# Kernel optimization log

Measured on AMD Instinct MI355X. Metric: run time of the kernel, lower is better.

Reference implementation:

```python
import jax, jax.numpy as jnp
import numpy as np

N, C, H = 384, 128, 4

def setup_inputs() -> dict:
    key = jax.random.key(0)
    ks = jax.random.split(key, 8)
    s = 1.0 / np.sqrt(C).astype(np.float32)
    pair = jax.random.normal(ks[0], (N, N, C), jnp.float32)
    mask = (jax.random.uniform(ks[1], (N, N)) > 0.5).astype(jnp.float32)
    return {
        'pair': pair,
        'mask': mask,
        'ln_w': jnp.ones((C,), jnp.float32),
        'ln_b': jnp.zeros((C,), jnp.float32),
        'bias_w': jax.random.normal(ks[2], (H, C), jnp.float32) * s,
        'q_w': jax.random.normal(ks[3], (C, C), jnp.float32) * s,
        'k_w': jax.random.normal(ks[4], (C, C), jnp.float32) * s,
        'v_w': jax.random.normal(ks[5], (C, C), jnp.float32) * s,
        'g_w': jax.random.normal(ks[6], (C, C), jnp.float32) * s,
        'o_w': jax.random.normal(ks[7], (C, C), jnp.float32) * s,
    }

def reference(pair, mask, ln_w, ln_b, bias_w, q_w, k_w, v_w, g_w, o_w):
    n, _, c = pair.shape
    h = bias_w.shape[0]
    d = c // h  # qkv_dim = c_pair // num_head
    # LayerNorm over channel dim (eps=1e-5, torch default)
    mu = jnp.mean(pair, axis=-1, keepdims=True)
    var = jnp.var(pair, axis=-1, keepdims=True)
    x = (pair - mu) * jax.lax.rsqrt(var + 1e-5) * ln_w + ln_b  # [N,N,C]
    # nonbatched pair bias: Linear(C->H), then permute(2,0,1) -> [H,N,N]
    bias = jnp.einsum('ijc,hc->hij', x, bias_w)
    # per-row (b) attention over keys j; Linear weight W: y = x @ W.T
    q = (x @ q_w.T).reshape(n, n, h, d)
    k = (x @ k_w.T).reshape(n, n, h, d)
    v = (x @ v_w.T).reshape(n, n, h, d)
    mask_bias = 1e9 * (mask - 1.0)  # [N,N]: -inf-like where masked per row b, key j
    logits = jnp.einsum('bihd,bjhd->bhij', q, k) * (1.0 / np.sqrt(d).astype(np.float32))
    logits = logits + bias[None, :, :, :] + mask_bias[:, None, None, :]
    w = jax.nn.softmax(logits, axis=-1)  # [N,H,N,N]
    o = jnp.einsum('bhij,bjhd->bihd', w, v).reshape(n, n, c)
    gate = jax.nn.sigmoid(x @ g_w.T)
    return (gate * o) @ o_w.T  # [N,N,C]
```

## Files before the change

### kernel.cpp

```cpp
#include <hip/hip_runtime.h>
#include <hip/hip_bf16.h>

#define NN 384
#define CC 128
#define HH 4
#define QK_SCALE 0.17677669529663687f

typedef float f32x4 __attribute__((ext_vector_type(4)));
typedef short s16x8 __attribute__((ext_vector_type(8)));
typedef short s16x4 __attribute__((ext_vector_type(4)));
typedef unsigned short u16;
typedef unsigned int u32;

__device__ __forceinline__ u16 f2b(float f) {
  union { float f; u32 u; } c; c.f = f;
  u32 u = c.u + 0x7FFFu + ((c.u >> 16) & 1u);
  return (u16)(u >> 16);
}
__device__ __forceinline__ u32 pack2(float a, float b) {
  return (u32)f2b(a) | ((u32)f2b(b) << 16);
}
__device__ __forceinline__ u32 pack2t(float a, float b) {
  union { float f; u32 u; } x, y; x.f = a; y.f = b;
  return (x.u >> 16) | (y.u & 0xFFFF0000u);
}
__device__ __forceinline__ float b2f_lo(u32 u) {
  union { u32 u; float f; } c; c.u = u << 16; return c.f;
}
__device__ __forceinline__ float b2f_hi(u32 u) {
  union { u32 u; float f; } c; c.u = u & 0xFFFF0000u; return c.f;
}
__device__ __forceinline__ s16x4 mk4(u32 a, u32 b) {
  union { u32 u[2]; s16x4 v; } c; c.u[0] = a; c.u[1] = b; return c.v;
}

#define MFMA32(a, b, c) __builtin_amdgcn_mfma_f32_16x16x32_bf16((a), (b), (c), 0, 0, 0)
#define MFMA16(a, b, c) __builtin_amdgcn_mfma_f32_16x16x16bf16_1k((a), (b), (c), 0, 0, 0)

__global__ __launch_bounds__(256) void k_ln_bias(
    const float* __restrict__ pair, const float* __restrict__ ln_w,
    const float* __restrict__ ln_b, const float* __restrict__ bias_w,
    const float* __restrict__ q_w, const float* __restrict__ k_w,
    const float* __restrict__ v_w, const float* __restrict__ g_w,
    const float* __restrict__ o_w, u16* __restrict__ xb,
    u16* __restrict__ biasf, u16* __restrict__ wqk, u16* __restrict__ wv,
    u16* __restrict__ wg, u16* __restrict__ wo) {
  if (blockIdx.x == 36864) {
    const int t = threadIdx.x;
    const float2* q2 = (const float2*)q_w;
    const float2* k2 = (const float2*)k_w;
    const float2* v2 = (const float2*)v_w;
    const float2* g2 = (const float2*)g_w;
    const float2* o2 = (const float2*)o_w;
    u32* dq = (u32*)wqk;
    u32* dk = (u32*)wqk + 8192;
    u32* dv = (u32*)wv;
    u32* dg = (u32*)wg;
    u32* dw = (u32*)wo;
    for (int i = t; i < 8192; i += 256) {
      float2 a = q2[i];
      dq[i] = pack2(a.x * QK_SCALE, a.y * QK_SCALE);
      a = k2[i]; dk[i] = pack2(a.x, a.y);
      a = v2[i]; dv[i] = pack2(a.x, a.y);
      a = g2[i]; dg[i] = pack2(a.x, a.y);
      a = o2[i]; dw[i] = pack2(a.x, a.y);
    }
    return;
  }
  const int wave = threadIdx.x >> 6;
  const int l = threadIdx.x & 63;
  const int p = blockIdx.x * 4 + wave;

  const float2 v = ((const float2*)pair)[(size_t)p * 64 + l];
  float s = v.x + v.y, sq = v.x * v.x + v.y * v.y;
#pragma unroll
  for (int off = 32; off >= 1; off >>= 1) {
    s += __shfl_xor(s, off);
    sq += __shfl_xor(sq, off);
  }
  const float mean = s * (1.0f / 128.0f);
  const float rstd = rsqrtf(sq * (1.0f / 128.0f) - mean * mean + 1e-5f);
  const float2 lw = ((const float2*)ln_w)[l];
  const float2 lb2 = ((const float2*)ln_b)[l];
  const float x0 = (v.x - mean) * rstd * lw.x + lb2.x;
  const float x1 = (v.y - mean) * rstd * lw.y + lb2.y;
  ((u32*)xb)[(size_t)p * 64 + l] = pack2(x0, x1);

  const int i = p / NN;
  const int j = p - i * NN;
  const int slot = ((j & 12) << 4) + ((i & 15) << 2) + (j & 3);
#pragma unroll
  for (int h = 0; h < HH; ++h) {
    const float2 bw = ((const float2*)bias_w)[h * 64 + l];
    float bp = x0 * bw.x + x1 * bw.y;
#pragma unroll
    for (int off = 32; off >= 1; off >>= 1) bp += __shfl_xor(bp, off);
    if (l == 0)
      biasf[(((h * 24 + (j >> 4)) * 24 + (i >> 4)) << 8) + slot] = f2b(bp);
  }
}

__global__ __launch_bounds__(256) void k_qkv(
    const u16* __restrict__ xb, const u16* __restrict__ wqk,
    const u16* __restrict__ wv, u16* __restrict__ qg, u16* __restrict__ kg,
    u16* __restrict__ vtf) {
  const int bid = blockIdx.x;
  const int b = bid / 6, jt6 = bid % 6;
  const int jrow0 = b * NN + jt6 * 64, jloc0 = jt6 * 64;
  const int t = threadIdx.x, w = t >> 6, l = t & 63;
  const int lr = l & 15, lg = l >> 4;
  const int n0 = w * 64;
  const int m0v = (w & 1) * 2;
  const int n0v = (w >> 1) * 64;

  f32x4 acc[4][4];
  f32x4 accv[2][4];
#pragma unroll
  for (int a = 0; a < 4; ++a)
#pragma unroll
    for (int c = 0; c < 4; ++c) acc[a][c] = (f32x4){0.f, 0.f, 0.f, 0.f};
#pragma unroll
  for (int a = 0; a < 2; ++a)
#pragma unroll
    for (int c = 0; c < 4; ++c) accv[a][c] = (f32x4){0.f, 0.f, 0.f, 0.f};

#pragma unroll
  for (int cs = 0; cs < 4; ++cs) {
    s16x8 bx[4];
#pragma unroll
    for (int ms = 0; ms < 4; ++ms)
      bx[ms] = *(const s16x8*)&xb[(size_t)(jrow0 + ms * 16 + lr) * CC +
                                  cs * 32 + lg * 8];
#pragma unroll
    for (int ns = 0; ns < 4; ++ns) {
      const s16x8 aW =
          *(const s16x8*)&wqk[(n0 + ns * 16 + lr) * CC + cs * 32 + lg * 8];
#pragma unroll
      for (int ms = 0; ms < 4; ++ms)
        acc[ns][ms] = MFMA32(aW, bx[ms], acc[ns][ms]);
      const s16x8 bV =
          *(const s16x8*)&wv[(n0v + ns * 16 + lr) * CC + cs * 32 + lg * 8];
#pragma unroll
      for (int mv = 0; mv < 2; ++mv)
        accv[mv][ns] = MFMA32(bx[m0v + mv], bV, accv[mv][ns]);
    }
  }

  {
    u16* base = (n0 >= 128) ? kg : qg;
    const int nb = n0 & 64;
#pragma unroll
    for (int ns = 0; ns < 4; ++ns) {
      const int nl = nb + ns * 16 + lg * 4;
      const int h = nl >> 5, d0 = nl & 31;
#pragma unroll
      for (int ms = 0; ms < 4; ++ms) {
        u32* dst = (u32*)(base + (size_t)(b * 4 + h) * 12288 +
                          (jloc0 + ms * 16 + lr) * 32 + d0);
        dst[0] = pack2(acc[ns][ms][0], acc[ns][ms][1]);
        dst[1] = pack2(acc[ns][ms][2], acc[ns][ms][3]);
      }
    }
  }

#pragma unroll
  for (int mv = 0; mv < 2; ++mv) {
#pragma unroll
    for (int ns = 0; ns < 4; ++ns) {
      const int n = n0v + ns * 16 + lr;
      const int h = n >> 5;
      const int dt = (n >> 4) & 1;
      const int j0 = jloc0 + (m0v + mv) * 16;
      u32* dst = (u32*)vtf +
                 ((((size_t)(b * 4 + h)) * 24 + (j0 >> 4)) * 2 + dt) * 128 +
                 l * 2;
      dst[0] = pack2(accv[mv][ns][0], accv[mv][ns][1]);
      dst[1] = pack2(accv[mv][ns][2], accv[mv][ns][3]);
    }
  }
}

__global__ __launch_bounds__(256) void k_attn(
    const u16* __restrict__ qg, const u16* __restrict__ kg,
    const u16* __restrict__ vtf, const u16* __restrict__ biasf,
    const float* __restrict__ mask, float* __restrict__ io) {
  __shared__ float mb[NN];
  const int bid = blockIdx.x;
  const int bh = bid >> 1, half = bid & 1;
  const int b = bh >> 2, h = bh & 3;
  const int t = threadIdx.x, w = t >> 6, l = t & 63;
  const int lr = l & 15, lg = l >> 4;

  for (int i = t; i < NN; i += 256) mb[i] = 1e9f * (mask[b * NN + i] - 1.0f);
  __syncthreads();

  const int q0 = half * 192 + w * 48, it0 = q0 >> 4;
  const u16* qb = qg + (size_t)bh * 12288;
  const u16* kb = kg + (size_t)bh * 12288;
  const u32* vt = (const u32*)vtf + (size_t)bh * 6144;
  const u32* bbf = (const u32*)biasf + (size_t)h * 73728;

  s16x8 bQ[3];
#pragma unroll
  for (int ms = 0; ms < 3; ++ms)
    bQ[ms] = *(const s16x8*)&qb[(q0 + ms * 16 + lr) * 32 + lg * 8];

  float mr[3], ls[3];
  f32x4 oa[3][2];
#pragma unroll
  for (int ms = 0; ms < 3; ++ms) {
    mr[ms] = -3.0e38f;
    ls[ms] = 0.f;
    oa[ms][0] = (f32x4){0.f, 0.f, 0.f, 0.f};
    oa[ms][1] = (f32x4){0.f, 0.f, 0.f, 0.f};
  }
  const f32x4 z4 = {0.f, 0.f, 0.f, 0.f};

#pragma unroll
  for (int kt = 0; kt < 6; ++kt) {
    s16x8 aK[4];
#pragma unroll
    for (int js = 0; js < 4; ++js)
      aK[js] = *(const s16x8*)&kb[(kt * 64 + js * 16 + lr) * 32 + lg * 8];
    u32 bw[3][4][2];
#pragma unroll
    for (int ms = 0; ms < 3; ++ms)
#pragma unroll
      for (int js = 0; js < 4; ++js) {
        const u32* p = bbf + ((kt * 4 + js) * 24 + it0 + ms) * 128 + l * 2;
        bw[ms][js][0] = p[0];
        bw[ms][js][1] = p[1];
      }
    s16x4 aV[4][2];
#pragma unroll
    for (int st = 0; st < 4; ++st)
#pragma unroll
      for (int ns = 0; ns < 2; ++ns)
        aV[st][ns] =
            *(const s16x4*)(vt + ((kt * 4 + st) * 2 + ns) * 128 + l * 2);

    f32x4 sT[3][4];
#pragma unroll
    for (int ms = 0; ms < 3; ++ms)
#pragma unroll
      for (int js = 0; js < 4; ++js) sT[ms][js] = MFMA32(aK[js], bQ[ms], z4);

#pragma unroll
    for (int js = 0; js < 4; ++js) {
      const int jb = kt * 64 + js * 16 + lg * 4;
      const f32x4 m4 = *(const f32x4*)&mb[jb];
#pragma unroll
      for (int ms = 0; ms < 3; ++ms) {
        const u32 b0 = bw[ms][js][0], b1 = bw[ms][js][1];
        sT[ms][js][0] += b2f_lo(b0) + m4[0];
        sT[ms][js][1] += b2f_hi(b0) + m4[1];
        sT[ms][js][2] += b2f_lo(b1) + m4[2];
        sT[ms][js][3] += b2f_hi(b1) + m4[3];
      }
    }

    u32 pk[3][4][2];
#pragma unroll
    for (int ms = 0; ms < 3; ++ms) {
      float tm = -3.0e38f;
#pragma unroll
      for (int js = 0; js < 4; ++js)
#pragma unroll
        for (int r = 0; r < 4; ++r) tm = fmaxf(tm, sT[ms][js][r]);
      tm = fmaxf(tm, __shfl_xor(tm, 16));
      tm = fmaxf(tm, __shfl_xor(tm, 32));
      const float nm = fmaxf(mr[ms], tm);
      const float sc = __expf(mr[ms] - nm);
      mr[ms] = nm;
      float ts = 0.f;
#pragma unroll
      for (int js = 0; js < 4; ++js)
#pragma unroll
        for (int r = 0; r < 4; ++r) {
          const float p = __expf(sT[ms][js][r] - nm);
          sT[ms][js][r] = p;
          ts += p;
        }
      ts += __shfl_xor(ts, 16);
      ts += __shfl_xor(ts, 32);
      ls[ms] = ls[ms] * sc + ts;
      oa[ms][0] *= sc;
      oa[ms][1] *= sc;
#pragma unroll
      for (int js = 0; js < 4; ++js) {
        pk[ms][js][0] = pack2t(sT[ms][js][0], sT[ms][js][1]);
        pk[ms][js][1] = pack2t(sT[ms][js][2], sT[ms][js][3]);
      }
    }

#pragma unroll
    for (int st = 0; st < 4; ++st) {
#pragma unroll
      for (int ms = 0; ms < 3; ++ms) {
        const s16x4 pb = mk4(pk[ms][st][0], pk[ms][st][1]);
#pragma unroll
        for (int ns = 0; ns < 2; ++ns)
          oa[ms][ns] = MFMA16(aV[st][ns], pb, oa[ms][ns]);
      }
    }
  }

#pragma unroll
  for (int ms = 0; ms < 3; ++ms) {
    const float inv = 1.0f / ls[ms];
    float* orow = io + ((size_t)b * NN + q0 + ms * 16 + lr) * CC + h * 32;
#pragma unroll
    for (int ns = 0; ns < 2; ++ns) {
      f32x4 vo = oa[ms][ns];
      vo *= inv;
      *(f32x4*)&orow[ns * 16 + lg * 4] = vo;
    }
  }
}

__global__ __launch_bounds__(256) void k_gate_out(
    const u16* __restrict__ xb, const u16* __restrict__ wg,
    const u16* __restrict__ wo, float* __restrict__ io) {
  const int bid = blockIdx.x;
  const int t = threadIdx.x, w = t >> 6, l = t & 63;
  const int lr = l & 15, lg = l >> 4;
  const int m0g = bid * 64 + w * 16;

  f32x4 a1[8];
#pragma unroll
  for (int ns = 0; ns < 8; ++ns) a1[ns] = (f32x4){0.f, 0.f, 0.f, 0.f};
#pragma unroll
  for (int cs = 0; cs < 4; ++cs) {
    const s16x8 bx =
        *(const s16x8*)&xb[(size_t)(m0g + lr) * CC + cs * 32 + lg * 8];
#pragma unroll
    for (int ns = 0; ns < 8; ++ns) {
      const s16x8 aW =
          *(const s16x8*)&wg[(ns * 16 + lr) * CC + cs * 32 + lg * 8];
      a1[ns] = MFMA32(aW, bx, a1[ns]);
    }
  }

  s16x4 pk2[8];
#pragma unroll
  for (int ns = 0; ns < 8; ++ns) {
    const f32x4 ov =
        *(const f32x4*)&io[(size_t)(m0g + lr) * CC + ns * 16 + lg * 4];
    float av[4];
#pragma unroll
    for (int r = 0; r < 4; ++r)
      av[r] = ov[r] / (1.0f + __expf(-a1[ns][r]));
    pk2[ns] = mk4(pack2(av[0], av[1]), pack2(av[2], av[3]));
  }

  f32x4 a2[8];
#pragma unroll
  for (int ns = 0; ns < 8; ++ns) a2[ns] = (f32x4){0.f, 0.f, 0.f, 0.f};
#pragma unroll
  for (int cs = 0; cs < 8; ++cs) {
#pragma unroll
    for (int ns = 0; ns < 8; ++ns) {
      const s16x4 aW2 =
          *(const s16x4*)&wo[(ns * 16 + lr) * CC + cs * 16 + lg * 4];
      a2[ns] = MFMA16(aW2, pk2[cs], a2[ns]);
    }
  }
#pragma unroll
  for (int ns = 0; ns < 8; ++ns)
    *(f32x4*)&io[(size_t)(m0g + lr) * CC + ns * 16 + lg * 4] = a2[ns];
}

extern "C" void kernel_launch(void* const* d_in, const int* in_sizes, int n_in,
                              void* d_out, int out_size, void* d_ws,
                              size_t ws_size, hipStream_t stream) {
  const float* pair = (const float*)d_in[0];
  const float* mask = (const float*)d_in[1];
  const float* ln_w = (const float*)d_in[2];
  const float* ln_b = (const float*)d_in[3];
  const float* bias_w = (const float*)d_in[4];
  const float* q_w = (const float*)d_in[5];
  const float* k_w = (const float*)d_in[6];
  const float* v_w = (const float*)d_in[7];
  const float* g_w = (const float*)d_in[8];
  const float* o_w = (const float*)d_in[9];

  char* wsb = (char*)d_ws;
  u16* xb = (u16*)wsb;
  u16* biasf = (u16*)(wsb + 37748736);
  u16* wqk = (u16*)(wsb + 38928384);
  u16* wv = (u16*)(wsb + 38993920);
  u16* wg = (u16*)(wsb + 39026688);
  u16* wo = (u16*)(wsb + 39059456);
  u16* qg = (u16*)(wsb + 39092224);
  u16* kg = (u16*)(wsb + 76840960);
  u16* vtf = (u16*)(wsb + 114589696);
  float* io = (float*)d_out;

  hipLaunchKernelGGL(k_ln_bias, dim3(NN * NN / 4 + 1), dim3(256), 0, stream,
                     pair, ln_w, ln_b, bias_w, q_w, k_w, v_w, g_w, o_w, xb,
                     biasf, wqk, wv, wg, wo);
  hipLaunchKernelGGL(k_qkv, dim3(NN * 6), dim3(256), 0, stream, xb, wqk, wv,
                     qg, kg, vtf);
  hipLaunchKernelGGL(k_attn, dim3(NN * HH * 2), dim3(256), 0, stream, qg, kg,
                     vtf, biasf, mask, io);
  hipLaunchKernelGGL(k_gate_out, dim3(NN * NN / 64), dim3(256), 0, stream, xb,
                     wg, wo, io);
}
```

Before: 620.5 us.

## Fuse QKV projection, attention, gating and output projection into one kernel

New measurement: 570.9 us. 1.09x faster.

```diff
diff --git a/kernel.cpp b/kernel.cpp
--- a/kernel.cpp
+++ b/kernel.cpp
@@ -5,6 +5,8 @@
 #define CC 128
 #define HH 4
 #define QK_SCALE 0.17677669529663687f
+#define LOG2E 1.4426950408889634f
+#define SMAX 20.0f
 
 typedef float f32x4 __attribute__((ext_vector_type(4)));
 typedef short s16x8 __attribute__((ext_vector_type(8)));
@@ -57,9 +59,10 @@
     u32* dv = (u32*)wv;
     u32* dg = (u32*)wg;
     u32* dw = (u32*)wo;
+    const float qs = QK_SCALE * LOG2E;
     for (int i = t; i < 8192; i += 256) {
       float2 a = q2[i];
-      dq[i] = pack2(a.x * QK_SCALE, a.y * QK_SCALE);
+      dq[i] = pack2(a.x * qs, a.y * qs);
       a = k2[i]; dk[i] = pack2(a.x, a.y);
       a = v2[i]; dv[i] = pack2(a.x, a.y);
       a = g2[i]; dg[i] = pack2(a.x, a.y);
@@ -96,278 +99,274 @@
 #pragma unroll
     for (int off = 32; off >= 1; off >>= 1) bp += __shfl_xor(bp, off);
     if (l == 0)
-      biasf[(((h * 24 + (j >> 4)) * 24 + (i >> 4)) << 8) + slot] = f2b(bp);
+      biasf[(((h * 24 + (j >> 4)) * 24 + (i >> 4)) << 8) + slot] =
+          f2b(bp * LOG2E);
   }
 }
 
-__global__ __launch_bounds__(256) void k_qkv(
+__global__ __launch_bounds__(256, 2) void k_mega(
     const u16* __restrict__ xb, const u16* __restrict__ wqk,
-    const u16* __restrict__ wv, u16* __restrict__ qg, u16* __restrict__ kg,
-    u16* __restrict__ vtf) {
+    const u16* __restrict__ wv, const u16* __restrict__ wg,
+    const u16* __restrict__ wo, const u16* __restrict__ biasf,
+    const float* __restrict__ mask, float* __restrict__ io) {
+  __shared__ u16 q_lds[192 * 40];
+  __shared__ u16 k_lds[192 * 40];
+  __shared__ u16 vt_lds[24 * 320];
+  __shared__ float mb[NN];
+
   const int bid = blockIdx.x;
-  const int b = bid / 6, jt6 = bid % 6;
-  const int jrow0 = b * NN + jt6 * 64, jloc0 = jt6 * 64;
+  const int b = bid >> 1, half = bid & 1;
   const int t = threadIdx.x, w = t >> 6, l = t & 63;
   const int lr = l & 15, lg = l >> 4;
-  const int n0 = w * 64;
-  const int m0v = (w & 1) * 2;
-  const int n0v = (w >> 1) * 64;
-
-  f32x4 acc[4][4];
-  f32x4 accv[2][4];
-#pragma unroll
-  for (int a = 0; a < 4; ++a)
-#pragma unroll
-    for (int c = 0; c < 4; ++c) acc[a][c] = (f32x4){0.f, 0.f, 0.f, 0.f};
-#pragma unroll
-  for (int a = 0; a < 2; ++a)
-#pragma unroll
-    for (int c = 0; c < 4; ++c) accv[a][c] = (f32x4){0.f, 0.f, 0.f, 0.f};
-
-#pragma unroll
-  for (int cs = 0; cs < 4; ++cs) {
-    s16x8 bx[4];
-#pragma unroll
-    for (int ms = 0; ms < 4; ++ms)
-      bx[ms] = *(const s16x8*)&xb[(size_t)(jrow0 + ms * 16 + lr) * CC +
-                                  cs * 32 + lg * 8];
-#pragma unroll
-    for (int ns = 0; ns < 4; ++ns) {
-      const s16x8 aW =
-          *(const s16x8*)&wqk[(n0 + ns * 16 + lr) * CC + cs * 32 + lg * 8];
-#pragma unroll
-      for (int ms = 0; ms < 4; ++ms)
-        acc[ns][ms] = MFMA32(aW, bx[ms], acc[ns][ms]);
-      const s16x8 bV =
-          *(const s16x8*)&wv[(n0v + ns * 16 + lr) * CC + cs * 32 + lg * 8];
-#pragma unroll
-      for (int mv = 0; mv < 2; ++mv)
-        accv[mv][ns] = MFMA32(bx[m0v + mv], bV, accv[mv][ns]);
+
+  for (int i = t; i < NN; i += 256)
+    mb[i] = LOG2E * 1e9f * (mask[b * NN + i] - 1.0f) - SMAX;
+
+  const int xrow_b = b * NN;
+  const int qrow_loc = half * 192 + w * 48;
+  const int itg0 = qrow_loc >> 4;
+  const f32x4 z4 = {0.f, 0.f, 0.f, 0.f};
+
+  u32 gos[3][HH][2][2];
+  s16x8 bQ[3];
+  float ls[3];
+  f32x4 oa[3][2];
+  u32 gatepk[3][2][2];
+
+#pragma unroll
+  for (int h = 0; h < HH; ++h) {
+    __syncthreads();
+
+    {
+      s16x8 bx[3][4];
+#pragma unroll
+      for (int ms = 0; ms < 3; ++ms)
+#pragma unroll
+        for (int cs = 0; cs < 4; ++cs)
+          bx[ms][cs] = *(const s16x8*)&xb[(size_t)(xrow_b + qrow_loc + ms * 16 +
+                                                   lr) * CC + cs * 32 + lg * 8];
+      f32x4 aq[2][3], ag[2][3];
+#pragma unroll
+      for (int ns = 0; ns < 2; ++ns)
+#pragma unroll
+        for (int ms = 0; ms < 3; ++ms) { aq[ns][ms] = z4; ag[ns][ms] = z4; }
+#pragma unroll
+      for (int cs = 0; cs < 4; ++cs) {
+#pragma unroll
+        for (int ns = 0; ns < 2; ++ns) {
+          const s16x8 aqw = *(const s16x8*)&wqk[(h * 32 + ns * 16 + lr) * CC +
+                                                cs * 32 + lg * 8];
+          const s16x8 agw = *(const s16x8*)&wg[(h * 32 + ns * 16 + lr) * CC +
+                                               cs * 32 + lg * 8];
+#pragma unroll
+          for (int ms = 0; ms < 3; ++ms) {
+            aq[ns][ms] = MFMA32(aqw, bx[ms][cs], aq[ns][ms]);
+            ag[ns][ms] = MFMA32(agw, bx[ms][cs], ag[ns][ms]);
+          }
+        }
+      }
+#pragma unroll
+      for (int ns = 0; ns < 2; ++ns)
+#pragma unroll
+        for (int ms = 0; ms < 3; ++ms) {
+          u32* dq = (u32*)q_lds + (w * 48 + ms * 16 + lr) * 20 + ns * 8 + lg * 2;
+          dq[0] = pack2(aq[ns][ms][0], aq[ns][ms][1]);
+          dq[1] = pack2(aq[ns][ms][2], aq[ns][ms][3]);
+          float sg[4];
+#pragma unroll
+          for (int r = 0; r < 4; ++r)
+            sg[r] = __builtin_amdgcn_rcpf(1.0f + __expf(-ag[ns][ms][r]));
+          gatepk[ms][ns][0] = pack2(sg[0], sg[1]);
+          gatepk[ms][ns][1] = pack2(sg[2], sg[3]);
+        }
+    }
+
+#pragma unroll
+    for (int ms = 0; ms < 3; ++ms) {
+      ls[ms] = 0.f;
+      oa[ms][0] = z4;
+      oa[ms][1] = z4;
+    }
+    const u32* bbf = (const u32*)biasf + (size_t)h * 73728;
+
+#pragma unroll
+    for (int c = 0; c < 2; ++c) {
+      if (c == 1) __syncthreads();
+      {
+        s16x8 bx2[3][4];
+#pragma unroll
+        for (int ms = 0; ms < 3; ++ms)
+#pragma unroll
+          for (int cs = 0; cs < 4; ++cs)
+            bx2[ms][cs] =
+                *(const s16x8*)&xb[(size_t)(xrow_b + c * 192 + w * 48 +
+                                            ms * 16 + lr) * CC + cs * 32 + lg * 8];
+        f32x4 ak2[2][3], av2[2][3];
+#pragma unroll
+        for (int ns = 0; ns < 2; ++ns)
+#pragma unroll
+          for (int ms = 0; ms < 3; ++ms) { ak2[ns][ms] = z4; av2[ns][ms] = z4; }
+#pragma unroll
+        for (int cs = 0; cs < 4; ++cs) {
+#pragma unroll
+          for (int ns = 0; ns < 2; ++ns) {
+            const s16x8 akw =
+                *(const s16x8*)&wqk[(128 + h * 32 + ns * 16 + lr) * CC +
+                                    cs * 32 + lg * 8];
+            const s16x8 avw = *(const s16x8*)&wv[(h * 32 + ns * 16 + lr) * CC +
+                                                 cs * 32 + lg * 8];
+#pragma unroll
+            for (int ms = 0; ms < 3; ++ms) {
+              ak2[ns][ms] = MFMA32(akw, bx2[ms][cs], ak2[ns][ms]);
+              av2[ns][ms] = MFMA32(avw, bx2[ms][cs], av2[ns][ms]);
+            }
+          }
+        }
+#pragma unroll
+        for (int ns = 0; ns < 2; ++ns)
+#pragma unroll
+          for (int ms = 0; ms < 3; ++ms) {
+            u32* dk = (u32*)k_lds + (w * 48 + ms * 16 + lr) * 20 + ns * 8 + lg * 2;
+            dk[0] = pack2(ak2[ns][ms][0], ak2[ns][ms][1]);
+            dk[1] = pack2(ak2[ns][ms][2], ak2[ns][ms][3]);
+            const int tt = (w * 3 + ms) * 2 + ns;
+#pragma unroll
+            for (int r = 0; r < 4; ++r)
+              vt_lds[tt * 320 + (lg * 4 + r) * 20 + lr] = f2b(av2[ns][ms][r]);
+          }
+      }
+      __syncthreads();
+
+      if (c == 0) {
+#pragma unroll
+        for (int ms = 0; ms < 3; ++ms)
+          bQ[ms] = *(const s16x8*)&q_lds[(w * 48 + ms * 16 + lr) * 40 + lg * 8];
+      }
+
+#pragma unroll
+      for (int ktl = 0; ktl < 3; ++ktl) {
+        const int ktg = c * 3 + ktl;
+        s16x8 aK[4];
+#pragma unroll
+        for (int js = 0; js < 4; ++js)
+          aK[js] =
+              *(const s16x8*)&k_lds[(ktl * 64 + js * 16 + lr) * 40 + lg * 8];
+        u32 bw[3][4][2];
+#pragma unroll
+        for (int ms = 0; ms < 3; ++ms)
+#pragma unroll
+          for (int js = 0; js < 4; ++js) {
+            const u32* p = bbf + ((ktg * 4 + js) * 24 + itg0 + ms) * 128 + l * 2;
+            bw[ms][js][0] = p[0];
+            bw[ms][js][1] = p[1];
+          }
+        s16x4 aV[4][2];
+#pragma unroll
+        for (int st = 0; st < 4; ++st)
+#pragma unroll
+          for (int ns = 0; ns < 2; ++ns)
+            aV[st][ns] = *(const s16x4*)&vt_lds[((ktl * 4 + st) * 2 + ns) * 320 +
+                                                lr * 20 + lg * 4];
+
+        f32x4 sT[3][4];
+#pragma unroll
+        for (int ms = 0; ms < 3; ++ms)
+#pragma unroll
+          for (int js = 0; js < 4; ++js) sT[ms][js] = MFMA32(aK[js], bQ[ms], z4);
+
+#pragma unroll
+        for (int js = 0; js < 4; ++js) {
+          const int jb = c * 192 + ktl * 64 + js * 16 + lg * 4;
+          const f32x4 m4 = *(const f32x4*)&mb[jb];
+#pragma unroll
+          for (int ms = 0; ms < 3; ++ms) {
+            const u32 b0 = bw[ms][js][0], b1 = bw[ms][js][1];
+            sT[ms][js][0] += b2f_lo(b0) + m4[0];
+            sT[ms][js][1] += b2f_hi(b0) + m4[1];
+            sT[ms][js][2] += b2f_lo(b1) + m4[2];
+            sT[ms][js][3] += b2f_hi(b1) + m4[3];
+          }
+        }
+
+        u32 pk[3][4][2];
+#pragma unroll
+        for (int ms = 0; ms < 3; ++ms) {
+          float ts = 0.f;
+#pragma unroll
+          for (int js = 0; js < 4; ++js)
+#pragma unroll
+            for (int r = 0; r < 4; ++r) {
+              const float p = exp2f(sT[ms][js][r]);
+              sT[ms][js][r] = p;
+              ts += p;
+            }
+          ts += __shfl_xor(ts, 16);
+          ts += __shfl_xor(ts, 32);
+          ls[ms] += ts;
+#pragma unroll
+          for (int js = 0; js < 4; ++js) {
+            pk[ms][js][0] = pack2t(sT[ms][js][0], sT[ms][js][1]);
+            pk[ms][js][1] = pack2t(sT[ms][js][2], sT[ms][js][3]);
+          }
+        }
+
+#pragma unroll
+        for (int st = 0; st < 4; ++st)
+#pragma unroll
+          for (int ms = 0; ms < 3; ++ms) {
+            const s16x4 pb = mk4(pk[ms][st][0], pk[ms][st][1]);
+#pragma unroll
+            for (int ns = 0; ns < 2; ++ns)
+              oa[ms][ns] = MFMA16(aV[st][ns], pb, oa[ms][ns]);
+          }
+      }
+    }
+
+#pragma unroll
+    for (int ms = 0; ms < 3; ++ms) {
+      const float inv = __builtin_amdgcn_rcpf(ls[ms]);
+#pragma unroll
+      for (int ns = 0; ns < 2; ++ns) {
+        const float g0 = b2f_lo(gatepk[ms][ns][0]);
+        const float g1 = b2f_hi(gatepk[ms][ns][0]);
+        const float g2 = b2f_lo(gatepk[ms][ns][1]);
+        const float g3 = b2f_hi(gatepk[ms][ns][1]);
+        const float v0 = oa[ms][ns][0] * inv * g0;
+        const float v1 = oa[ms][ns][1] * inv * g1;
+        const float v2 = oa[ms][ns][2] * inv * g2;
+        const float v3 = oa[ms][ns][3] * inv * g3;
+        gos[ms][h][ns][0] = pack2(v0, v1);
+        gos[ms][h][ns][1] = pack2(v2, v3);
+      }
     }
   }
 
-  {
-    u16* base = (n0 >= 128) ? kg : qg;
-    const int nb = n0 & 64;
-#pragma unroll
-    for (int ns = 0; ns < 4; ++ns) {
-      const int nl = nb + ns * 16 + lg * 4;
-      const int h = nl >> 5, d0 = nl & 31;
-#pragma unroll
-      for (int ms = 0; ms < 4; ++ms) {
-        u32* dst = (u32*)(base + (size_t)(b * 4 + h) * 12288 +
-                          (jloc0 + ms * 16 + lr) * 32 + d0);
-        dst[0] = pack2(acc[ns][ms][0], acc[ns][ms][1]);
-        dst[1] = pack2(acc[ns][ms][2], acc[ns][ms][3]);
-      }
-    }
+  f32x4 acc2[8][3];
+#pragma unroll
+  for (int ns2 = 0; ns2 < 8; ++ns2)
+#pragma unroll
+    for (int ms = 0; ms < 3; ++ms) acc2[ns2][ms] = z4;
+#pragma unroll
+  for (int h2 = 0; h2 < HH; ++h2)
+#pragma unroll
+    for (int ns = 0; ns < 2; ++ns)
+#pragma unroll
+      for (int ns2 = 0; ns2 < 8; ++ns2) {
+        const s16x4 aW = *(const s16x4*)&wo[(ns2 * 16 + lr) * CC + h2 * 32 +
+                                            ns * 16 + lg * 4];
+#pragma unroll
+        for (int ms = 0; ms < 3; ++ms)
+          acc2[ns2][ms] =
+              MFMA16(aW, mk4(gos[ms][h2][ns][0], gos[ms][h2][ns][1]),
+                     acc2[ns2][ms]);
+      }
+#pragma unroll
+  for (int ms = 0; ms < 3; ++ms) {
+    float* orow = io + (size_t)(xrow_b + qrow_loc + ms * 16 + lr) * CC;
+#pragma unroll
+    for (int ns2 = 0; ns2 < 8; ++ns2)
+      *(f32x4*)&orow[ns2 * 16 + lg * 4] = acc2[ns2][ms];
   }
-
-#pragma unroll
-  for (int mv = 0; mv < 2; ++mv) {
-#pragma unroll
-    for (int ns = 0; ns < 4; ++ns) {
-      const int n = n0v + ns * 16 + lr;
-      const int h = n >> 5;
-      const int dt = (n >> 4) & 1;
-      const int j0 = jloc0 + (m0v + mv) * 16;
-      u32* dst = (u32*)vtf +
-                 ((((size_t)(b * 4 + h)) * 24 + (j0 >> 4)) * 2 + dt) * 128 +
-                 l * 2;
-      dst[0] = pack2(accv[mv][ns][0], accv[mv][ns][1]);
-      dst[1] = pack2(accv[mv][ns][2], accv[mv][ns][3]);
-    }
-  }
-}
-
-__global__ __launch_bounds__(256) void k_attn(
-    const u16* __restrict__ qg, const u16* __restrict__ kg,
-    const u16* __restrict__ vtf, const u16* __restrict__ biasf,
-    const float* __restrict__ mask, float* __restrict__ io) {
-  __shared__ float mb[NN];
-  const int bid = blockIdx.x;
-  const int bh = bid >> 1, half = bid & 1;
-  const int b = bh >> 2, h = bh & 3;
-  const int t = threadIdx.x, w = t >> 6, l = t & 63;
-  const int lr = l & 15, lg = l >> 4;
-
-  for (int i = t; i < NN; i += 256) mb[i] = 1e9f * (mask[b * NN + i] - 1.0f);
-  __syncthreads();
-
-  const int q0 = half * 192 + w * 48, it0 = q0 >> 4;
-  const u16* qb = qg + (size_t)bh * 12288;
-  const u16* kb = kg + (size_t)bh * 12288;
-  const u32* vt = (const u32*)vtf + (size_t)bh * 6144;
-  const u32* bbf = (const u32*)biasf + (size_t)h * 73728;
-
-  s16x8 bQ[3];
-#pragma unroll
-  for (int ms = 0; ms < 3; ++ms)
-    bQ[ms] = *(const s16x8*)&qb[(q0 + ms * 16 + lr) * 32 + lg * 8];
-
-  float mr[3], ls[3];
-  f32x4 oa[3][2];
-#pragma unroll
-  for (int ms = 0; ms < 3; ++ms) {
-    mr[ms] = -3.0e38f;
-    ls[ms] = 0.f;
-    oa[ms][0] = (f32x4){0.f, 0.f, 0.f, 0.f};
-    oa[ms][1] = (f32x4){0.f, 0.f, 0.f, 0.f};
-  }
-  const f32x4 z4 = {0.f, 0.f, 0.f, 0.f};
-
-#pragma unroll
-  for (int kt = 0; kt < 6; ++kt) {
-    s16x8 aK[4];
-#pragma unroll
-    for (int js = 0; js < 4; ++js)
-      aK[js] = *(const s16x8*)&kb[(kt * 64 + js * 16 + lr) * 32 + lg * 8];
-    u32 bw[3][4][2];
-#pragma unroll
-    for (int ms = 0; ms < 3; ++ms)
-#pragma unroll
-      for (int js = 0; js < 4; ++js) {
-        const u32* p = bbf + ((kt * 4 + js) * 24 + it0 + ms) * 128 + l * 2;
-        bw[ms][js][0] = p[0];
-        bw[ms][js][1] = p[1];
-      }
-    s16x4 aV[4][2];
-#pragma unroll
-    for (int st = 0; st < 4; ++st)
-#pragma unroll
-      for (int ns = 0; ns < 2; ++ns)
-        aV[st][ns] =
-            *(const s16x4*)(vt + ((kt * 4 + st) * 2 + ns) * 128 + l * 2);
-
-    f32x4 sT[3][4];
-#pragma unroll
-    for (int ms = 0; ms < 3; ++ms)
-#pragma unroll
-      for (int js = 0; js < 4; ++js) sT[ms][js] = MFMA32(aK[js], bQ[ms], z4);
-
-#pragma unroll
-    for (int js = 0; js < 4; ++js) {
-      const int jb = kt * 64 + js * 16 + lg * 4;
-      const f32x4 m4 = *(const f32x4*)&mb[jb];
-#pragma unroll
-      for (int ms = 0; ms < 3; ++ms) {
-        const u32 b0 = bw[ms][js][0], b1 = bw[ms][js][1];
-        sT[ms][js][0] += b2f_lo(b0) + m4[0];
-        sT[ms][js][1] += b2f_hi(b0) + m4[1];
-        sT[ms][js][2] += b2f_lo(b1) + m4[2];
-        sT[ms][js][3] += b2f_hi(b1) + m4[3];
-      }
-    }
-
-    u32 pk[3][4][2];
-#pragma unroll
-    for (int ms = 0; ms < 3; ++ms) {
-      float tm = -3.0e38f;
-#pragma unroll
-      for (int js = 0; js < 4; ++js)
-#pragma unroll
-        for (int r = 0; r < 4; ++r) tm = fmaxf(tm, sT[ms][js][r]);
-      tm = fmaxf(tm, __shfl_xor(tm, 16));
-      tm = fmaxf(tm, __shfl_xor(tm, 32));
-      const float nm = fmaxf(mr[ms], tm);
-      const float sc = __expf(mr[ms] - nm);
-      mr[ms] = nm;
-      float ts = 0.f;
-#pragma unroll
-      for (int js = 0; js < 4; ++js)
-#pragma unroll
-        for (int r = 0; r < 4; ++r) {
-          const float p = __expf(sT[ms][js][r] - nm);
-          sT[ms][js][r] = p;
-          ts += p;
-        }
-      ts += __shfl_xor(ts, 16);
-      ts += __shfl_xor(ts, 32);
-      ls[ms] = ls[ms] * sc + ts;
-      oa[ms][0] *= sc;
-      oa[ms][1] *= sc;
-#pragma unroll
-      for (int js = 0; js < 4; ++js) {
-        pk[ms][js][0] = pack2t(sT[ms][js][0], sT[ms][js][1]);
-        pk[ms][js][1] = pack2t(sT[ms][js][2], sT[ms][js][3]);
-      }
-    }
-
-#pragma unroll
-    for (int st = 0; st < 4; ++st) {
-#pragma unroll
-      for (int ms = 0; ms < 3; ++ms) {
-        const s16x4 pb = mk4(pk[ms][st][0], pk[ms][st][1]);
-#pragma unroll
-        for (int ns = 0; ns < 2; ++ns)
-          oa[ms][ns] = MFMA16(aV[st][ns], pb, oa[ms][ns]);
-      }
-    }
-  }
-
-#pragma unroll
-  for (int ms = 0; ms < 3; ++ms) {
-    const float inv = 1.0f / ls[ms];
-    float* orow = io + ((size_t)b * NN + q0 + ms * 16 + lr) * CC + h * 32;
-#pragma unroll
-    for (int ns = 0; ns < 2; ++ns) {
-      f32x4 vo = oa[ms][ns];
-      vo *= inv;
-      *(f32x4*)&orow[ns * 16 + lg * 4] = vo;
-    }
-  }
-}
-
-__global__ __launch_bounds__(256) void k_gate_out(
-    const u16* __restrict__ xb, const u16* __restrict__ wg,
-    const u16* __restrict__ wo, float* __restrict__ io) {
-  const int bid = blockIdx.x;
-  const int t = threadIdx.x, w = t >> 6, l = t & 63;
-  const int lr = l & 15, lg = l >> 4;
-  const int m0g = bid * 64 + w * 16;
-
-  f32x4 a1[8];
-#pragma unroll
-  for (int ns = 0; ns < 8; ++ns) a1[ns] = (f32x4){0.f, 0.f, 0.f, 0.f};
-#pragma unroll
-  for (int cs = 0; cs < 4; ++cs) {
-    const s16x8 bx =
-        *(const s16x8*)&xb[(size_t)(m0g + lr) * CC + cs * 32 + lg * 8];
-#pragma unroll
-    for (int ns = 0; ns < 8; ++ns) {
-      const s16x8 aW =
-          *(const s16x8*)&wg[(ns * 16 + lr) * CC + cs * 32 + lg * 8];
-      a1[ns] = MFMA32(aW, bx, a1[ns]);
-    }
-  }
-
-  s16x4 pk2[8];
-#pragma unroll
-  for (int ns = 0; ns < 8; ++ns) {
-    const f32x4 ov =
-        *(const f32x4*)&io[(size_t)(m0g + lr) * CC + ns * 16 + lg * 4];
-    float av[4];
-#pragma unroll
-    for (int r = 0; r < 4; ++r)
-      av[r] = ov[r] / (1.0f + __expf(-a1[ns][r]));
-    pk2[ns] = mk4(pack2(av[0], av[1]), pack2(av[2], av[3]));
-  }
-
-  f32x4 a2[8];
-#pragma unroll
-  for (int ns = 0; ns < 8; ++ns) a2[ns] = (f32x4){0.f, 0.f, 0.f, 0.f};
-#pragma unroll
-  for (int cs = 0; cs < 8; ++cs) {
-#pragma unroll
-    for (int ns = 0; ns < 8; ++ns) {
-      const s16x4 aW2 =
-          *(const s16x4*)&wo[(ns * 16 + lr) * CC + cs * 16 + lg * 4];
-      a2[ns] = MFMA16(aW2, pk2[cs], a2[ns]);
-    }
-  }
-#pragma unroll
-  for (int ns = 0; ns < 8; ++ns)
-    *(f32x4*)&io[(size_t)(m0g + lr) * CC + ns * 16 + lg * 4] = a2[ns];
 }
 
 extern "C" void kernel_launch(void* const* d_in, const int* in_sizes, int n_in,
@@ -391,18 +390,11 @@
   u16* wv = (u16*)(wsb + 38993920);
   u16* wg = (u16*)(wsb + 39026688);
   u16* wo = (u16*)(wsb + 39059456);
-  u16* qg = (u16*)(wsb + 39092224);
-  u16* kg = (u16*)(wsb + 76840960);
-  u16* vtf = (u16*)(wsb + 114589696);
   float* io = (float*)d_out;
 
   hipLaunchKernelGGL(k_ln_bias, dim3(NN * NN / 4 + 1), dim3(256), 0, stream,
                      pair, ln_w, ln_b, bias_w, q_w, k_w, v_w, g_w, o_w, xb,
                      biasf, wqk, wv, wg, wo);
-  hipLaunchKernelGGL(k_qkv, dim3(NN * 6), dim3(256), 0, stream, xb, wqk, wv,
-                     qg, kg, vtf);
-  hipLaunchKernelGGL(k_attn, dim3(NN * HH * 2), dim3(256), 0, stream, qg, kg,
-                     vtf, biasf, mask, io);
-  hipLaunchKernelGGL(k_gate_out, dim3(NN * NN / 64), dim3(256), 0, stream, xb,
-                     wg, wo, io);
-}
+  hipLaunchKernelGGL(k_mega, dim3(NN * 2), dim3(256), 0, stream, xb, wqk, wv,
+                     wg, wo, biasf, mask, io);
+}
```
